# Kernel optimization log

Hardware: AMD Instinct MI355X
Metric: run time of the kernel (lower is better)

Reference implementation:

```python
import jax, jax.numpy as jnp
import numpy as np

P = 128   # input_size == proj_size
H = 512   # hidden_size
L = 6     # num_layers
STEPS = 32


def setup_inputs() -> dict:
    key = jax.random.key(0)
    ks = jax.random.split(key, 8)
    B, T = 512, 512
    scale = 1.0 / np.sqrt(H)
    s = lambda k, shape: (jax.random.normal(k, shape, jnp.float32) * scale)
    return {
        "x": jax.random.normal(ks[0], (B, T, P), jnp.float32),
        "W_ih": s(ks[1], (L, 4 * H, P)),
        "W_hh": s(ks[2], (L, 4 * H, P)),
        "b_ih": s(ks[3], (L, 4 * H)),
        "b_hh": s(ks[4], (L, 4 * H)),
        "W_hr": s(ks[5], (L, P, H)),
        "W_fc": s(ks[6], (P, P)),
        "b_fc": s(ks[7], (P,)),
    }


def _cell(xt, h, c, Wih, Whh, b, Whr):
    # PyTorch LSTM gate order: i, f, g, o ; proj: h = (o*tanh(c)) @ Whr^T
    gates = xt @ Wih.T + h @ Whh.T + b  # [B, 4H]
    i, f, g, o = jnp.split(gates, 4, axis=-1)
    c = jax.nn.sigmoid(f) * c + jax.nn.sigmoid(i) * jnp.tanh(g)
    h_full = jax.nn.sigmoid(o) * jnp.tanh(c)  # [B, H]
    h = h_full @ Whr.T  # [B, P]
    return h, c


def reference(x, W_ih, W_hh, b_ih, b_hh, W_hr, W_fc, b_fc):
    B = x.shape[0]
    b = b_ih + b_hh  # [L, 4H]
    inp = jnp.swapaxes(x, 0, 1)  # time-major [T, B, P]

    # --- encode: run full sequence through the 6-layer stack, keep final (h, c) ---
    hs, cs = [], []
    for l in range(L):
        def step(carry, xt, l=l):
            h, c = carry
            h, c = _cell(xt, h, c, W_ih[l], W_hh[l], b[l], W_hr[l])
            return (h, c), h
        init = (jnp.zeros((B, P), x.dtype), jnp.zeros((B, H), x.dtype))
        (h, c), inp = jax.lax.scan(step, init, inp)
        hs.append(h)
        cs.append(c)
    hs = jnp.stack(hs)  # [L, B, P]
    cs = jnp.stack(cs)  # [L, B, H]

    zero = jnp.zeros((B, P), x.dtype)
    def dec(carry, _):
        hs, cs = carry
        xt = zero
        nh, nc = [], []
        for l in range(L):
            h, c = _cell(xt, hs[l], cs[l], W_ih[l], W_hh[l], b[l], W_hr[l])
            nh.append(h)
            nc.append(c)
            xt = h
        out = jax.nn.sigmoid(xt) @ W_fc.T + b_fc  # sigmoid THEN fc, as in source
        return (jnp.stack(nh), jnp.stack(nc)), out

    _, zs = jax.lax.scan(dec, (hs, cs), None, length=STEPS)  # [32, B, P]
    return jnp.swapaxes(zs, 0, 1)  # [B, 32, P]
```

## Files before the change

kernel.cpp:

```cpp
#include <hip/hip_runtime.h>

typedef short s8v __attribute__((ext_vector_type(8)));
typedef float f4v __attribute__((ext_vector_type(4)));
typedef unsigned long long ull;

#define NLAYER 6
#define HID    512
#define PROJ   128
#define SEQT   512
#define BATCH  512
#define DSTEPS 32
#define TOTS   (SEQT + DSTEPS)
#define NG     2048
#define BC     64
#define NCHUNK (BATCH / BC)
#define NUNIT  (NLAYER * NCHUNK)
#define RINGP  4
#define PP_SH  8192
#define FSTRIDE 16

#define GFRAGS (NLAYER * 128 * 8 * 64)
#define PFRAGS (NLAYER * 8 * 16 * 64)
#define FFRAGS (8 * 4 * 64)
#define NFLAGS (NUNIT * 4 * FSTRIDE)

static __device__ __forceinline__ unsigned short f2b(float f) {
    union { float f; unsigned int u; } v; v.f = f;
    unsigned int r = v.u + 0x7fffu + ((v.u >> 16) & 1u);
    return (unsigned short)(r >> 16);
}
static __device__ __forceinline__ float b2f(unsigned short s) {
    union { float f; unsigned int u; } v; v.u = ((unsigned int)s) << 16;
    return v.f;
}
static __device__ __forceinline__ float sigf(float x) {
    x = fminf(fmaxf(x, -30.f), 30.f);
    return 1.f / (1.f + __expf(-x));
}
static __device__ __forceinline__ float tanh_fast(float x) {
    x = fminf(fmaxf(x, -15.f), 15.f);
    float t = __expf(-2.f * x);
    return (1.f - t) / (1.f + t);
}
static __device__ __forceinline__ f4v mfma16(s8v a, s8v b, f4v c) {
    return __builtin_amdgcn_mfma_f32_16x16x32_bf16(a, b, c, 0, 0, 0);
}
static __device__ __forceinline__ ull ald(const ull* p) {
    return __hip_atomic_load(p, __ATOMIC_RELAXED, __HIP_MEMORY_SCOPE_AGENT);
}
static __device__ __forceinline__ void spin_ge(unsigned* p, unsigned v) {
    while (__hip_atomic_load(p, __ATOMIC_RELAXED, __HIP_MEMORY_SCOPE_AGENT) < v)
        __builtin_amdgcn_s_sleep(2);
}
static __device__ __forceinline__ ull pk4(float a, float b, float c, float d) {
    return (ull)f2b(a) | ((ull)f2b(b) << 16) | ((ull)f2b(c) << 32) | ((ull)f2b(d) << 48);
}
static __device__ __forceinline__ float rsum4(ull v0, ull v1, ull v2, ull v3, int sh) {
    return b2f((unsigned short)(v0 >> sh)) + b2f((unsigned short)(v1 >> sh))
         + b2f((unsigned short)(v2 >> sh)) + b2f((unsigned short)(v3 >> sh));
}

__global__ __launch_bounds__(256) void lstm_prepack(
    const float* __restrict__ Wih, const float* __restrict__ Whh,
    const float* __restrict__ bih, const float* __restrict__ bhh,
    const float* __restrict__ Whr, const float* __restrict__ Wfc,
    const float* __restrict__ bfcin,
    unsigned short* __restrict__ gB, unsigned short* __restrict__ pB,
    unsigned short* __restrict__ fB, float* __restrict__ bsum,
    float* __restrict__ bfc, unsigned int* __restrict__ flags)
{
    int tid = blockIdx.x * 256 + threadIdx.x;

    if (tid < GFRAGS) {
        const int lane = tid & 63;
        int rest = tid >> 6;
        const int kt = rest & 7;   rest >>= 3;
        const int nt = rest & 127; rest >>= 7;
        const int l  = rest;
        const int n  = nt * 16 + (lane & 15);
        const int kb = kt * 32 + (lane >> 4) * 8;
        const float* src = (kb < 128)
            ? (Wih + ((size_t)l * NG + n) * PROJ + kb)
            : (Whh + ((size_t)l * NG + n) * PROJ + (kb - 128));
        unsigned short o[8];
        #pragma unroll
        for (int e = 0; e < 8; ++e) o[e] = f2b(src[e]);
        *(s8v*)(gB + (size_t)tid * 8) = *(const s8v*)o;
        return;
    }
    tid -= GFRAGS;
    if (tid < PFRAGS) {
        const int lane = tid & 63;
        int rest = tid >> 6;
        const int kt = rest & 15; rest >>= 4;
        const int nt = rest & 7;  rest >>= 3;
        const int l  = rest;
        const int n  = nt * 16 + (lane & 15);
        const int kb = kt * 32 + (lane >> 4) * 8;
        const float* src = Whr + ((size_t)l * PROJ + n) * HID + kb;
        unsigned short o[8];
        #pragma unroll
        for (int e = 0; e < 8; ++e) o[e] = f2b(src[e]);
        *(s8v*)(pB + (size_t)tid * 8) = *(const s8v*)o;
        return;
    }
    tid -= PFRAGS;
    if (tid < FFRAGS) {
        const int lane = tid & 63;
        int rest = tid >> 6;
        const int kt = rest & 3;
        const int nt = rest >> 2;
        const int n  = nt * 16 + (lane & 15);
        const int kb = kt * 32 + (lane >> 4) * 8;
        const float* src = Wfc + (size_t)n * PROJ + kb;
        unsigned short o[8];
        #pragma unroll
        for (int e = 0; e < 8; ++e) o[e] = f2b(src[e]);
        *(s8v*)(fB + (size_t)tid * 8) = *(const s8v*)o;
        return;
    }
    tid -= FFRAGS;
    if (tid < NLAYER * NG) { bsum[tid] = bih[tid] + bhh[tid]; return; }
    tid -= NLAYER * NG;
    if (tid < PROJ) { bfc[tid] = bfcin[tid]; return; }
    tid -= PROJ;
    if (tid < NFLAGS) { flags[tid] = 0u; return; }
}

__global__ __launch_bounds__(512) void lstm_main(
    const float* __restrict__ x,
    const unsigned short* __restrict__ gB,
    const unsigned short* __restrict__ pB,
    const unsigned short* __restrict__ fB,
    const float* __restrict__ bsum,
    const float* __restrict__ bfc,
    unsigned int* __restrict__ flags,
    unsigned short* __restrict__ pp,
    float* __restrict__ out)
{
    const int xcd  = blockIdx.x & 7;
    const int slot = blockIdx.x >> 3;
    const int uo   = slot >> 2;
    const int sub  = slot & 3;
    const int unit = xcd * 6 + uo;
    const int l    = unit >> 3;
    const int bb   = (unit & 7) * BC;

    __shared__ __align__(16) unsigned short xcat[64][264];
    __shared__ __align__(16) unsigned short hfullA[64][136];
    __shared__ __align__(16) unsigned short pslab[2048 * 8];

    const int tid  = threadIdx.x;
    const int lane = tid & 63;
    const int w    = tid >> 6;
    const int u    = sub * 8 + w;
    const int mrow = lane & 15;
    const int kgrp = lane >> 4;

    for (int i = tid; i < 64 * 264; i += 512) ((unsigned short*)xcat)[i] = 0;

    const s8v* gfrag = (const s8v*)gB;
    const s8v* pfrag = (const s8v*)pB;
    const s8v* ffrag = (const s8v*)fB;

    s8v wreg[4][8];
    #pragma unroll
    for (int g = 0; g < 4; ++g)
      #pragma unroll
      for (int kt = 0; kt < 8; ++kt)
        wreg[g][kt] = gfrag[(((size_t)l * 128 + g * 32 + u) * 8 + kt) * 64 + lane];

    float bias[4];
    #pragma unroll
    for (int g = 0; g < 4; ++g)
        bias[g] = bsum[l * NG + g * HID + u * 16 + mrow];

    for (int i = tid; i < 2048; i += 512) {
        const int nt = i >> 8, ktl = (i >> 6) & 3, ln = i & 63;
        ((s8v*)pslab)[i] = pfrag[(((size_t)l * 8 + nt) * 16 + sub * 4 + ktl) * 64 + ln];
    }

    f4v cst[4];
    #pragma unroll
    for (int mt = 0; mt < 4; ++mt) cst[mt] = (f4v){0.f, 0.f, 0.f, 0.f};

    unsigned int* tg = flags;

    __syncthreads();

    #pragma unroll 1
    for (int s = 0; s < TOTS; ++s) {
        if (s > 0 && tid < 4)
            spin_ge(&tg[(unit * 4 + tid) * FSTRIDE], (unsigned)s);
        if (l > 0 && tid >= 64 && tid < 68)
            spin_ge(&tg[((unit - NCHUNK) * 4 + (tid - 64)) * FSTRIDE], (unsigned)(s + 1));
        if (l < NLAYER - 1 && s >= RINGP && tid >= 128 && tid < 132)
            spin_ge(&tg[((unit + NCHUNK) * 4 + (tid - 128)) * FSTRIDE], (unsigned)(s - RINGP + 1));
        __syncthreads();

        if (l > 0) {
            const ull* bu = (const ull*)(pp + ((size_t)((unit - NCHUNK) * RINGP + (s & 3)) * 4) * PP_SH);
            const ull* bh = (const ull*)(pp + ((size_t)(unit * RINGP + ((s - 1) & 3)) * 4) * PP_SH);
            if (s > 0) {
                #pragma unroll
                for (int k = 0; k < 4; ++k) {
                    const int idx = k * 512 + tid;
                    const int m = idx >> 5, p4 = idx & 31;
                    const ull a0 = ald(bu + idx),        a1 = ald(bu + 2048 + idx);
                    const ull a2 = ald(bu + 4096 + idx), a3 = ald(bu + 6144 + idx);
                    const ull b0 = ald(bh + idx),        b1 = ald(bh + 2048 + idx);
                    const ull b2 = ald(bh + 4096 + idx), b3 = ald(bh + 6144 + idx);
                    *(ull*)&xcat[m][p4 * 4] = pk4(
                        rsum4(a0, a1, a2, a3, 0),  rsum4(a0, a1, a2, a3, 16),
                        rsum4(a0, a1, a2, a3, 32), rsum4(a0, a1, a2, a3, 48));
                    *(ull*)&xcat[m][128 + p4 * 4] = pk4(
                        rsum4(b0, b1, b2, b3, 0),  rsum4(b0, b1, b2, b3, 16),
                        rsum4(b0, b1, b2, b3, 32), rsum4(b0, b1, b2, b3, 48));
                }
            } else {
                #pragma unroll
                for (int k = 0; k < 4; ++k) {
                    const int idx = k * 512 + tid;
                    const int m = idx >> 5, p4 = idx & 31;
                    const ull a0 = ald(bu + idx),        a1 = ald(bu + 2048 + idx);
                    const ull a2 = ald(bu + 4096 + idx), a3 = ald(bu + 6144 + idx);
                    *(ull*)&xcat[m][p4 * 4] = pk4(
                        rsum4(a0, a1, a2, a3, 0),  rsum4(a0, a1, a2, a3, 16),
                        rsum4(a0, a1, a2, a3, 32), rsum4(a0, a1, a2, a3, 48));
                }
            }
        } else {
            if (s < SEQT) {
                #pragma unroll
                for (int k = 0; k < 4; ++k) {
                    const int f = k * 512 + tid;
                    const int m = f >> 5, q4 = f & 31;
                    const float4 v = *(const float4*)(x + (((size_t)(bb + m)) * SEQT + s) * PROJ + q4 * 4);
                    *(ull*)&xcat[m][q4 * 4] = pk4(v.x, v.y, v.z, v.w);
                }
            } else if (s == SEQT) {
                #pragma unroll
                for (int k = 0; k < 4; ++k) {
                    const int f = k * 512 + tid;
                    *(ull*)&xcat[f >> 5][(f & 31) * 4] = 0ull;
                }
            }
            if (s > 0) {
                const ull* bh = (const ull*)(pp + ((size_t)(unit * RINGP + ((s - 1) & 3)) * 4) * PP_SH);
                #pragma unroll
                for (int k = 0; k < 4; ++k) {
                    const int idx = k * 512 + tid;
                    const int m = idx >> 5, p4 = idx & 31;
                    const ull b0 = ald(bh + idx),        b1 = ald(bh + 2048 + idx);
                    const ull b2 = ald(bh + 4096 + idx), b3 = ald(bh + 6144 + idx);
                    *(ull*)&xcat[m][128 + p4 * 4] = pk4(
                        rsum4(b0, b1, b2, b3, 0),  rsum4(b0, b1, b2, b3, 16),
                        rsum4(b0, b1, b2, b3, 32), rsum4(b0, b1, b2, b3, 48));
                }
            }
        }
        __syncthreads();

        #pragma unroll
        for (int mt = 0; mt < 4; ++mt) {
            f4v a0 = (f4v){bias[0], bias[0], bias[0], bias[0]};
            f4v a1 = (f4v){bias[1], bias[1], bias[1], bias[1]};
            f4v a2 = (f4v){bias[2], bias[2], bias[2], bias[2]};
            f4v a3 = (f4v){bias[3], bias[3], bias[3], bias[3]};
            #pragma unroll
            for (int kt = 0; kt < 8; ++kt) {
                const s8v a = *(const s8v*)&xcat[mt * 16 + mrow][kt * 32 + kgrp * 8];
                a0 = mfma16(a, wreg[0][kt], a0);
                a1 = mfma16(a, wreg[1][kt], a1);
                a2 = mfma16(a, wreg[2][kt], a2);
                a3 = mfma16(a, wreg[3][kt], a3);
            }
            f4v cv = cst[mt];
            #pragma unroll
            for (int r = 0; r < 4; ++r) {
                const float cn = sigf(a1[r]) * cv[r] + sigf(a0[r]) * tanh_fast(a2[r]);
                const float hf = sigf(a3[r]) * tanh_fast(cn);
                cv[r] = cn;
                hfullA[mt * 16 + kgrp * 4 + r][w * 16 + mrow] = f2b(hf);
            }
            cst[mt] = cv;
        }
        __syncthreads();

        {
            f4v pacc[4];
            #pragma unroll
            for (int mt = 0; mt < 4; ++mt) pacc[mt] = (f4v){0.f, 0.f, 0.f, 0.f};
            #pragma unroll
            for (int ktl = 0; ktl < 4; ++ktl) {
                const s8v wf = ((const s8v*)pslab)[(w * 4 + ktl) * 64 + lane];
                #pragma unroll
                for (int mt = 0; mt < 4; ++mt) {
                    const s8v hf = *(const s8v*)&hfullA[mt * 16 + mrow][ktl * 32 + kgrp * 8];
                    pacc[mt] = mfma16(wf, hf, pacc[mt]);
                }
            }
            unsigned short* dst = pp + ((size_t)(unit * RINGP + (s & 3)) * 4 + sub) * PP_SH;
            #pragma unroll
            for (int mt = 0; mt < 4; ++mt) {
                ull* p8 = (ull*)(dst + (mt * 16 + mrow) * 128 + w * 16 + kgrp * 4);
                __hip_atomic_store(p8, pk4(pacc[mt][0], pacc[mt][1], pacc[mt][2], pacc[mt][3]),
                                   __ATOMIC_RELAXED, __HIP_MEMORY_SCOPE_AGENT);
            }
        }
        __syncthreads();
        if (tid == 0)
            __hip_atomic_store(&tg[(unit * 4 + sub) * FSTRIDE], (unsigned)(s + 1),
                               __ATOMIC_RELAXED, __HIP_MEMORY_SCOPE_AGENT);

        if (l == NLAYER - 1 && s >= SEQT) {
            if (tid < 4) spin_ge(&tg[(unit * 4 + tid) * FSTRIDE], (unsigned)(s + 1));
            __syncthreads();
            const ull* bh = (const ull*)(pp + ((size_t)(unit * RINGP + (s & 3)) * 4) * PP_SH);
            #pragma unroll
            for (int k = 0; k < 4; ++k) {
                const int idx = k * 512 + tid;
                const int m = idx >> 5, p4 = idx & 31;
                const ull b0 = ald(bh + idx),        b1 = ald(bh + 2048 + idx);
                const ull b2 = ald(bh + 4096 + idx), b3 = ald(bh + 6144 + idx);
                *(ull*)&hfullA[m][p4 * 4] = pk4(
                    sigf(rsum4(b0, b1, b2, b3, 0)),  sigf(rsum4(b0, b1, b2, b3, 16)),
                    sigf(rsum4(b0, b1, b2, b3, 32)), sigf(rsum4(b0, b1, b2, b3, 48)));
            }
            __syncthreads();
            const float bv = bfc[w * 16 + mrow];
            f4v facc[4];
            #pragma unroll
            for (int mt = 0; mt < 4; ++mt) facc[mt] = (f4v){bv, bv, bv, bv};
            #pragma unroll
            for (int kt = 0; kt < 4; ++kt) {
                const s8v bf = ffrag[((size_t)w * 4 + kt) * 64 + lane];
                #pragma unroll
                for (int mt = 0; mt < 4; ++mt) {
                    const s8v a = *(const s8v*)&hfullA[mt * 16 + mrow][kt * 32 + kgrp * 8];
                    facc[mt] = mfma16(a, bf, facc[mt]);
                }
            }
            const int td = s - SEQT;
            #pragma unroll
            for (int mt = 0; mt < 4; ++mt)
                #pragma unroll
                for (int r = 0; r < 4; ++r)
                    out[(((size_t)(bb + mt * 16 + kgrp * 4 + r)) * DSTEPS + td) * PROJ
                        + w * 16 + mrow] = facc[mt][r];
        }
    }
}

extern "C" void kernel_launch(void* const* d_in, const int* in_sizes, int n_in,
                              void* d_out, int out_size, void* d_ws, size_t ws_size,
                              hipStream_t stream)
{
    const float* x    = (const float*)d_in[0];
    const float* Wih  = (const float*)d_in[1];
    const float* Whh  = (const float*)d_in[2];
    const float* bih  = (const float*)d_in[3];
    const float* bhh  = (const float*)d_in[4];
    const float* Whr  = (const float*)d_in[5];
    const float* Wfc  = (const float*)d_in[6];
    const float* bfcv = (const float*)d_in[7];

    char* ws = (char*)d_ws;
    size_t off = 0;
    auto alloc = [&](size_t b) { char* p = ws + off; off += (b + 255) & ~(size_t)255; return p; };
    unsigned short* gB  = (unsigned short*)alloc((size_t)GFRAGS * 16);
    unsigned short* pB  = (unsigned short*)alloc((size_t)PFRAGS * 16);
    unsigned short* fB  = (unsigned short*)alloc((size_t)FFRAGS * 16);
    float* bsum         = (float*)alloc((size_t)NLAYER * NG * 4);
    float* bfc          = (float*)alloc((size_t)PROJ * 4);
    unsigned int* flags = (unsigned int*)alloc((size_t)NFLAGS * 4);
    unsigned short* pp  = (unsigned short*)alloc((size_t)NUNIT * RINGP * 4 * PP_SH * 2);
    if (off > ws_size) return;

    const int total = GFRAGS + PFRAGS + FFRAGS + NLAYER * NG + PROJ + NFLAGS;
    lstm_prepack<<<(total + 255) / 256, 256, 0, stream>>>(
        Wih, Whh, bih, bhh, Whr, Wfc, bfcv, gB, pB, fB, bsum, bfc, flags);
    lstm_main<<<NUNIT * 4, 512, 0, stream>>>(
        x, gB, pB, fB, bsum, bfc, flags, pp, (float*)d_out);
}
```

Baseline: 7.086 ms.

## Split each timestep into two batch-half phases with separate readiness flags

Each time step is split into two phases, each handling half of the 64-row batch chunk, and each phase has its own set of progress flags. Downstream layers and the next step can begin on the first half as soon as it is published, instead of waiting for the whole chunk. This deepens the wavefront pipeline across layers and sub-blocks. The cost is twice as many barriers, spin-waits and flag stores per step, and each phase does half the MFMA work, which lowers per-phase efficiency.

New measurement: 7.094 ms. About the same (+0.1%).

```diff
diff --git a/kernel.cpp b/kernel.cpp
--- a/kernel.cpp
+++ b/kernel.cpp
@@ -18,11 +18,12 @@
 #define RINGP  4
 #define PP_SH  8192
 #define FSTRIDE 16
+#define TAGHALF (NUNIT * 4 * FSTRIDE)
 
 #define GFRAGS (NLAYER * 128 * 8 * 64)
 #define PFRAGS (NLAYER * 8 * 16 * 64)
 #define FFRAGS (8 * 4 * 64)
-#define NFLAGS (NUNIT * 4 * FSTRIDE)
+#define NFLAGS (2 * TAGHALF)
 
 static __device__ __forceinline__ unsigned short f2b(float f) {
     union { float f; unsigned int u; } v; v.f = f;
@@ -190,131 +191,142 @@
 
     #pragma unroll 1
     for (int s = 0; s < TOTS; ++s) {
-        if (s > 0 && tid < 4)
-            spin_ge(&tg[(unit * 4 + tid) * FSTRIDE], (unsigned)s);
-        if (l > 0 && tid >= 64 && tid < 68)
-            spin_ge(&tg[((unit - NCHUNK) * 4 + (tid - 64)) * FSTRIDE], (unsigned)(s + 1));
-        if (l < NLAYER - 1 && s >= RINGP && tid >= 128 && tid < 132)
-            spin_ge(&tg[((unit + NCHUNK) * 4 + (tid - 128)) * FSTRIDE], (unsigned)(s - RINGP + 1));
-        __syncthreads();
-
-        if (l > 0) {
-            const ull* bu = (const ull*)(pp + ((size_t)((unit - NCHUNK) * RINGP + (s & 3)) * 4) * PP_SH);
-            const ull* bh = (const ull*)(pp + ((size_t)(unit * RINGP + ((s - 1) & 3)) * 4) * PP_SH);
-            if (s > 0) {
-                #pragma unroll
-                for (int k = 0; k < 4; ++k) {
-                    const int idx = k * 512 + tid;
-                    const int m = idx >> 5, p4 = idx & 31;
-                    const ull a0 = ald(bu + idx),        a1 = ald(bu + 2048 + idx);
-                    const ull a2 = ald(bu + 4096 + idx), a3 = ald(bu + 6144 + idx);
-                    const ull b0 = ald(bh + idx),        b1 = ald(bh + 2048 + idx);
-                    const ull b2 = ald(bh + 4096 + idx), b3 = ald(bh + 6144 + idx);
-                    *(ull*)&xcat[m][p4 * 4] = pk4(
-                        rsum4(a0, a1, a2, a3, 0),  rsum4(a0, a1, a2, a3, 16),
-                        rsum4(a0, a1, a2, a3, 32), rsum4(a0, a1, a2, a3, 48));
-                    *(ull*)&xcat[m][128 + p4 * 4] = pk4(
-                        rsum4(b0, b1, b2, b3, 0),  rsum4(b0, b1, b2, b3, 16),
-                        rsum4(b0, b1, b2, b3, 32), rsum4(b0, b1, b2, b3, 48));
+        #pragma unroll
+        for (int ph = 0; ph < 2; ++ph) {
+            unsigned int* tgP = tg + ph * TAGHALF;
+
+            if (s > 0 && tid < 4)
+                spin_ge(&tgP[(unit * 4 + tid) * FSTRIDE], (unsigned)s);
+            if (l > 0 && tid >= 64 && tid < 68)
+                spin_ge(&tgP[((unit - NCHUNK) * 4 + (tid - 64)) * FSTRIDE], (unsigned)(s + 1));
+            if (l < NLAYER - 1 && s >= RINGP && tid >= 128 && tid < 132)
+                spin_ge(&tgP[((unit + NCHUNK) * 4 + (tid - 128)) * FSTRIDE], (unsigned)(s - RINGP + 1));
+            __syncthreads();
+
+            if (l > 0) {
+                const ull* bu = (const ull*)(pp + ((size_t)((unit - NCHUNK) * RINGP + (s & 3)) * 4) * PP_SH);
+                const ull* bh = (const ull*)(pp + ((size_t)(unit * RINGP + ((s - 1) & 3)) * 4) * PP_SH);
+                if (s > 0) {
+                    #pragma unroll
+                    for (int kk = 0; kk < 2; ++kk) {
+                        const int idx = (ph * 2 + kk) * 512 + tid;
+                        const int m = idx >> 5, p4 = idx & 31;
+                        const ull a0 = ald(bu + idx),        a1 = ald(bu + 2048 + idx);
+                        const ull a2 = ald(bu + 4096 + idx), a3 = ald(bu + 6144 + idx);
+                        const ull b0 = ald(bh + idx),        b1 = ald(bh + 2048 + idx);
+                        const ull b2 = ald(bh + 4096 + idx), b3 = ald(bh + 6144 + idx);
+                        *(ull*)&xcat[m][p4 * 4] = pk4(
+                            rsum4(a0, a1, a2, a3, 0),  rsum4(a0, a1, a2, a3, 16),
+                            rsum4(a0, a1, a2, a3, 32), rsum4(a0, a1, a2, a3, 48));
+                        *(ull*)&xcat[m][128 + p4 * 4] = pk4(
+                            rsum4(b0, b1, b2, b3, 0),  rsum4(b0, b1, b2, b3, 16),
+                            rsum4(b0, b1, b2, b3, 32), rsum4(b0, b1, b2, b3, 48));
+                    }
+                } else {
+                    #pragma unroll
+                    for (int kk = 0; kk < 2; ++kk) {
+                        const int idx = (ph * 2 + kk) * 512 + tid;
+                        const int m = idx >> 5, p4 = idx & 31;
+                        const ull a0 = ald(bu + idx),        a1 = ald(bu + 2048 + idx);
+                        const ull a2 = ald(bu + 4096 + idx), a3 = ald(bu + 6144 + idx);
+                        *(ull*)&xcat[m][p4 * 4] = pk4(
+                            rsum4(a0, a1, a2, a3, 0),  rsum4(a0, a1, a2, a3, 16),
+                            rsum4(a0, a1, a2, a3, 32), rsum4(a0, a1, a2, a3, 48));
+                    }
                 }
             } else {
-                #pragma unroll
-                for (int k = 0; k < 4; ++k) {
-                    const int idx = k * 512 + tid;
-                    const int m = idx >> 5, p4 = idx & 31;
-                    const ull a0 = ald(bu + idx),        a1 = ald(bu + 2048 + idx);
-                    const ull a2 = ald(bu + 4096 + idx), a3 = ald(bu + 6144 + idx);
-                    *(ull*)&xcat[m][p4 * 4] = pk4(
-                        rsum4(a0, a1, a2, a3, 0),  rsum4(a0, a1, a2, a3, 16),
-                        rsum4(a0, a1, a2, a3, 32), rsum4(a0, a1, a2, a3, 48));
-                }
-            }
-        } else {
-            if (s < SEQT) {
-                #pragma unroll
-                for (int k = 0; k < 4; ++k) {
-                    const int f = k * 512 + tid;
-                    const int m = f >> 5, q4 = f & 31;
-                    const float4 v = *(const float4*)(x + (((size_t)(bb + m)) * SEQT + s) * PROJ + q4 * 4);
-                    *(ull*)&xcat[m][q4 * 4] = pk4(v.x, v.y, v.z, v.w);
-                }
-            } else if (s == SEQT) {
-                #pragma unroll
-                for (int k = 0; k < 4; ++k) {
-                    const int f = k * 512 + tid;
-                    *(ull*)&xcat[f >> 5][(f & 31) * 4] = 0ull;
-                }
-            }
-            if (s > 0) {
-                const ull* bh = (const ull*)(pp + ((size_t)(unit * RINGP + ((s - 1) & 3)) * 4) * PP_SH);
-                #pragma unroll
-                for (int k = 0; k < 4; ++k) {
-                    const int idx = k * 512 + tid;
-                    const int m = idx >> 5, p4 = idx & 31;
-                    const ull b0 = ald(bh + idx),        b1 = ald(bh + 2048 + idx);
-                    const ull b2 = ald(bh + 4096 + idx), b3 = ald(bh + 6144 + idx);
-                    *(ull*)&xcat[m][128 + p4 * 4] = pk4(
-                        rsum4(b0, b1, b2, b3, 0),  rsum4(b0, b1, b2, b3, 16),
-                        rsum4(b0, b1, b2, b3, 32), rsum4(b0, b1, b2, b3, 48));
-                }
-            }
+                if (s < SEQT) {
+                    #pragma unroll
+                    for (int kk = 0; kk < 2; ++kk) {
+                        const int f = (ph * 2 + kk) * 512 + tid;
+                        const int m = f >> 5, q4 = f & 31;
+                        const float4 v = *(const float4*)(x + (((size_t)(bb + m)) * SEQT + s) * PROJ + q4 * 4);
+                        *(ull*)&xcat[m][q4 * 4] = pk4(v.x, v.y, v.z, v.w);
+                    }
+                } else if (s == SEQT) {
+                    #pragma unroll
+                    for (int kk = 0; kk < 2; ++kk) {
+                        const int f = (ph * 2 + kk) * 512 + tid;
+                        *(ull*)&xcat[f >> 5][(f & 31) * 4] = 0ull;
+                    }
+                }
+                if (s > 0) {
+                    const ull* bh = (const ull*)(pp + ((size_t)(unit * RINGP + ((s - 1) & 3)) * 4) * PP_SH);
+                    #pragma unroll
+                    for (int kk = 0; kk < 2; ++kk) {
+                        const int idx = (ph * 2 + kk) * 512 + tid;
+                        const int m = idx >> 5, p4 = idx & 31;
+                        const ull b0 = ald(bh + idx),        b1 = ald(bh + 2048 + idx);
+                        const ull b2 = ald(bh + 4096 + idx), b3 = ald(bh + 6144 + idx);
+                        *(ull*)&xcat[m][128 + p4 * 4] = pk4(
+                            rsum4(b0, b1, b2, b3, 0),  rsum4(b0, b1, b2, b3, 16),
+                            rsum4(b0, b1, b2, b3, 32), rsum4(b0, b1, b2, b3, 48));
+                    }
+                }
+            }
+            __syncthreads();
+
+            #pragma unroll
+            for (int mm = 0; mm < 2; ++mm) {
+                const int mt = ph * 2 + mm;
+                f4v a0 = (f4v){bias[0], bias[0], bias[0], bias[0]};
+                f4v a1 = (f4v){bias[1], bias[1], bias[1], bias[1]};
+                f4v a2 = (f4v){bias[2], bias[2], bias[2], bias[2]};
+                f4v a3 = (f4v){bias[3], bias[3], bias[3], bias[3]};
+                #pragma unroll
+                for (int kt = 0; kt < 8; ++kt) {
+                    const s8v a = *(const s8v*)&xcat[mt * 16 + mrow][kt * 32 + kgrp * 8];
+                    a0 = mfma16(a, wreg[0][kt], a0);
+                    a1 = mfma16(a, wreg[1][kt], a1);
+                    a2 = mfma16(a, wreg[2][kt], a2);
+                    a3 = mfma16(a, wreg[3][kt], a3);
+                }
+                f4v cv = cst[mt];
+                #pragma unroll
+                for (int r = 0; r < 4; ++r) {
+                    const float cn = sigf(a1[r]) * cv[r] + sigf(a0[r]) * tanh_fast(a2[r]);
+                    const float hf = sigf(a3[r]) * tanh_fast(cn);
+                    cv[r] = cn;
+                    hfullA[mt * 16 + kgrp * 4 + r][w * 16 + mrow] = f2b(hf);
+                }
+                cst[mt] = cv;
+            }
+            __syncthreads();
+
+            {
+                f4v pacc[2];
+                pacc[0] = (f4v){0.f, 0.f, 0.f, 0.f};
+                pacc[1] = (f4v){0.f, 0.f, 0.f, 0.f};
+                #pragma unroll
+                for (int ktl = 0; ktl < 4; ++ktl) {
+                    const s8v wf = ((const s8v*)pslab)[(w * 4 + ktl) * 64 + lane];
+                    #pragma unroll
+                    for (int mm = 0; mm < 2; ++mm) {
+                        const int mt = ph * 2 + mm;
+                        const s8v hf = *(const s8v*)&hfullA[mt * 16 + mrow][ktl * 32 + kgrp * 8];
+                        pacc[mm] = mfma16(wf, hf, pacc[mm]);
+                    }
+                }
+                unsigned short* dst = pp + ((size_t)(unit * RINGP + (s & 3)) * 4 + sub) * PP_SH;
+                #pragma unroll
+                for (int mm = 0; mm < 2; ++mm) {
+                    const int mt = ph * 2 + mm;
+                    ull* p8 = (ull*)(dst + (mt * 16 + mrow) * 128 + w * 16 + kgrp * 4);
+                    __hip_atomic_store(p8, pk4(pacc[mm][0], pacc[mm][1], pacc[mm][2], pacc[mm][3]),
+                                       __ATOMIC_RELAXED, __HIP_MEMORY_SCOPE_AGENT);
+                }
+            }
+            __syncthreads();
+            if (tid == 0)
+                __hip_atomic_store(&tgP[(unit * 4 + sub) * FSTRIDE], (unsigned)(s + 1),
+                                   __ATOMIC_RELAXED, __HIP_MEMORY_SCOPE_AGENT);
         }
-        __syncthreads();
-
-        #pragma unroll
-        for (int mt = 0; mt < 4; ++mt) {
-            f4v a0 = (f4v){bias[0], bias[0], bias[0], bias[0]};
-            f4v a1 = (f4v){bias[1], bias[1], bias[1], bias[1]};
-            f4v a2 = (f4v){bias[2], bias[2], bias[2], bias[2]};
-            f4v a3 = (f4v){bias[3], bias[3], bias[3], bias[3]};
-            #pragma unroll
-            for (int kt = 0; kt < 8; ++kt) {
-                const s8v a = *(const s8v*)&xcat[mt * 16 + mrow][kt * 32 + kgrp * 8];
-                a0 = mfma16(a, wreg[0][kt], a0);
-                a1 = mfma16(a, wreg[1][kt], a1);
-                a2 = mfma16(a, wreg[2][kt], a2);
-                a3 = mfma16(a, wreg[3][kt], a3);
-            }
-            f4v cv = cst[mt];
-            #pragma unroll
-            for (int r = 0; r < 4; ++r) {
-                const float cn = sigf(a1[r]) * cv[r] + sigf(a0[r]) * tanh_fast(a2[r]);
-                const float hf = sigf(a3[r]) * tanh_fast(cn);
-                cv[r] = cn;
-                hfullA[mt * 16 + kgrp * 4 + r][w * 16 + mrow] = f2b(hf);
-            }
-            cst[mt] = cv;
-        }
-        __syncthreads();
-
-        {
-            f4v pacc[4];
-            #pragma unroll
-            for (int mt = 0; mt < 4; ++mt) pacc[mt] = (f4v){0.f, 0.f, 0.f, 0.f};
-            #pragma unroll
-            for (int ktl = 0; ktl < 4; ++ktl) {
-                const s8v wf = ((const s8v*)pslab)[(w * 4 + ktl) * 64 + lane];
-                #pragma unroll
-                for (int mt = 0; mt < 4; ++mt) {
-                    const s8v hf = *(const s8v*)&hfullA[mt * 16 + mrow][ktl * 32 + kgrp * 8];
-                    pacc[mt] = mfma16(wf, hf, pacc[mt]);
-                }
-            }
-            unsigned short* dst = pp + ((size_t)(unit * RINGP + (s & 3)) * 4 + sub) * PP_SH;
-            #pragma unroll
-            for (int mt = 0; mt < 4; ++mt) {
-                ull* p8 = (ull*)(dst + (mt * 16 + mrow) * 128 + w * 16 + kgrp * 4);
-                __hip_atomic_store(p8, pk4(pacc[mt][0], pacc[mt][1], pacc[mt][2], pacc[mt][3]),
-                                   __ATOMIC_RELAXED, __HIP_MEMORY_SCOPE_AGENT);
-            }
-        }
-        __syncthreads();
-        if (tid == 0)
-            __hip_atomic_store(&tg[(unit * 4 + sub) * FSTRIDE], (unsigned)(s + 1),
-                               __ATOMIC_RELAXED, __HIP_MEMORY_SCOPE_AGENT);
 
         if (l == NLAYER - 1 && s >= SEQT) {
-            if (tid < 4) spin_ge(&tg[(unit * 4 + tid) * FSTRIDE], (unsigned)(s + 1));
+            if (tid < 8) {
+                unsigned int* tp = tg + (tid >> 2) * TAGHALF;
+                spin_ge(&tp[(unit * 4 + (tid & 3)) * FSTRIDE], (unsigned)(s + 1));
+            }
             __syncthreads();
             const ull* bh = (const ull*)(pp + ((size_t)(unit * RINGP + (s & 3)) * 4) * PP_SH);
             #pragma unroll
```

## Vectorize partial-projection exchange with 16-byte coherent loads/stores in new layout

Applied to the files above, without the earlier changes.

Changes the layout of the per-step projection partial sums in the global ring buffer so that each thread writes two 16-byte stores and each reader issues eight 16-byte loads, replacing many 8-byte atomic loads and stores. The loads use inline asm with cache-bypass bits and explicit waitcnts, so the h-path loads overlap the reduction of the upper-layer input. It also adds a min-blocks hint to launch_bounds. The aim is to cut latency on the critical inter-block communication path, at the cost of hand-written asm memory ordering that relies on the sc0/sc1 semantics for coherence.

New measurement: 6.956 ms. No clear change (-1.8%).

```diff
diff --git a/kernel.cpp b/kernel.cpp
--- a/kernel.cpp
+++ b/kernel.cpp
@@ -2,6 +2,7 @@
 
 typedef short s8v __attribute__((ext_vector_type(8)));
 typedef float f4v __attribute__((ext_vector_type(4)));
+typedef unsigned int u4v __attribute__((ext_vector_type(4)));
 typedef unsigned long long ull;
 
 #define NLAYER 6
@@ -29,9 +30,11 @@
     unsigned int r = v.u + 0x7fffu + ((v.u >> 16) & 1u);
     return (unsigned short)(r >> 16);
 }
-static __device__ __forceinline__ float b2f(unsigned short s) {
-    union { float f; unsigned int u; } v; v.u = ((unsigned int)s) << 16;
-    return v.f;
+static __device__ __forceinline__ float blo(unsigned int u) {
+    union { unsigned int x; float f; } v; v.x = u << 16; return v.f;
+}
+static __device__ __forceinline__ float bhi(unsigned int u) {
+    union { unsigned int x; float f; } v; v.x = u & 0xffff0000u; return v.f;
 }
 static __device__ __forceinline__ float sigf(float x) {
     x = fminf(fmaxf(x, -30.f), 30.f);
@@ -45,9 +48,6 @@
 static __device__ __forceinline__ f4v mfma16(s8v a, s8v b, f4v c) {
     return __builtin_amdgcn_mfma_f32_16x16x32_bf16(a, b, c, 0, 0, 0);
 }
-static __device__ __forceinline__ ull ald(const ull* p) {
-    return __hip_atomic_load(p, __ATOMIC_RELAXED, __HIP_MEMORY_SCOPE_AGENT);
-}
 static __device__ __forceinline__ void spin_ge(unsigned* p, unsigned v) {
     while (__hip_atomic_load(p, __ATOMIC_RELAXED, __HIP_MEMORY_SCOPE_AGENT) < v)
         __builtin_amdgcn_s_sleep(2);
@@ -55,9 +55,62 @@
 static __device__ __forceinline__ ull pk4(float a, float b, float c, float d) {
     return (ull)f2b(a) | ((ull)f2b(b) << 16) | ((ull)f2b(c) << 32) | ((ull)f2b(d) << 48);
 }
-static __device__ __forceinline__ float rsum4(ull v0, ull v1, ull v2, ull v3, int sh) {
-    return b2f((unsigned short)(v0 >> sh)) + b2f((unsigned short)(v1 >> sh))
-         + b2f((unsigned short)(v2 >> sh)) + b2f((unsigned short)(v3 >> sh));
+static __device__ __forceinline__ ull red4(unsigned a0, unsigned a1, unsigned a2, unsigned a3,
+                                           unsigned b0, unsigned b1, unsigned b2, unsigned b3) {
+    return pk4(blo(a0) + blo(a1) + blo(a2) + blo(a3),
+               bhi(a0) + bhi(a1) + bhi(a2) + bhi(a3),
+               blo(b0) + blo(b1) + blo(b2) + blo(b3),
+               bhi(b0) + bhi(b1) + bhi(b2) + bhi(b3));
+}
+static __device__ __forceinline__ ull red4s(unsigned a0, unsigned a1, unsigned a2, unsigned a3,
+                                            unsigned b0, unsigned b1, unsigned b2, unsigned b3) {
+    return pk4(sigf(blo(a0) + blo(a1) + blo(a2) + blo(a3)),
+               sigf(bhi(a0) + bhi(a1) + bhi(a2) + bhi(a3)),
+               sigf(blo(b0) + blo(b1) + blo(b2) + blo(b3)),
+               sigf(bhi(b0) + bhi(b1) + bhi(b2) + bhi(b3)));
+}
+static __device__ __forceinline__ u4v mk4(ull a, ull b) {
+    u4v r; r.x = (unsigned)a; r.y = (unsigned)(a >> 32);
+    r.z = (unsigned)b; r.w = (unsigned)(b >> 32); return r;
+}
+
+#define LD8_BODY(WAITSTR) \
+    const ull* p0 = b;        const ull* p1 = b + 2;    \
+    const ull* p2 = b + 2048; const ull* p3 = b + 2050; \
+    const ull* p4 = b + 4096; const ull* p5 = b + 4098; \
+    const ull* p6 = b + 6144; const ull* p7 = b + 6146; \
+    asm volatile( \
+        "global_load_dwordx4 %0, %8, off sc0 sc1\n\t"  \
+        "global_load_dwordx4 %1, %9, off sc0 sc1\n\t"  \
+        "global_load_dwordx4 %2, %10, off sc0 sc1\n\t" \
+        "global_load_dwordx4 %3, %11, off sc0 sc1\n\t" \
+        "global_load_dwordx4 %4, %12, off sc0 sc1\n\t" \
+        "global_load_dwordx4 %5, %13, off sc0 sc1\n\t" \
+        "global_load_dwordx4 %6, %14, off sc0 sc1\n\t" \
+        "global_load_dwordx4 %7, %15, off sc0 sc1"     \
+        WAITSTR \
+        : "=&v"(r0), "=&v"(r1), "=&v"(r2), "=&v"(r3), \
+          "=&v"(r4), "=&v"(r5), "=&v"(r6), "=&v"(r7)  \
+        : "v"(p0), "v"(p1), "v"(p2), "v"(p3), "v"(p4), "v"(p5), "v"(p6), "v"(p7) \
+        : "memory")
+
+static __device__ __forceinline__ void ld8nw(const ull* b,
+    u4v& r0, u4v& r1, u4v& r2, u4v& r3, u4v& r4, u4v& r5, u4v& r6, u4v& r7) {
+    LD8_BODY("");
+}
+static __device__ __forceinline__ void ld8w8(const ull* b,
+    u4v& r0, u4v& r1, u4v& r2, u4v& r3, u4v& r4, u4v& r5, u4v& r6, u4v& r7) {
+    LD8_BODY("\n\ts_waitcnt vmcnt(8)");
+}
+static __device__ __forceinline__ void ld8w0(const ull* b,
+    u4v& r0, u4v& r1, u4v& r2, u4v& r3, u4v& r4, u4v& r5, u4v& r6, u4v& r7) {
+    LD8_BODY("\n\ts_waitcnt vmcnt(0)");
+}
+static __device__ __forceinline__ void st16x2(ull* p, u4v v01, u4v v23) {
+    asm volatile("global_store_dwordx4 %0, %2, off sc0 sc1\n\t"
+                 "global_store_dwordx4 %1, %3, off sc0 sc1\n\t"
+                 "s_waitcnt vmcnt(0)"
+                 :: "v"(p), "v"(p + 2), "v"(v01), "v"(v23) : "memory");
 }
 
 __global__ __launch_bounds__(256) void lstm_prepack(
@@ -127,7 +180,7 @@
     if (tid < NFLAGS) { flags[tid] = 0u; return; }
 }
 
-__global__ __launch_bounds__(512) void lstm_main(
+__global__ __launch_bounds__(512, 2) void lstm_main(
     const float* __restrict__ x,
     const unsigned short* __restrict__ gB,
     const unsigned short* __restrict__ pB,
@@ -156,6 +209,8 @@
     const int u    = sub * 8 + w;
     const int mrow = lane & 15;
     const int kgrp = lane >> 4;
+    const int mrc  = tid >> 5;
+    const int pc4  = (tid & 31) * 4;
 
     for (int i = tid; i < 64 * 264; i += 512) ((unsigned short*)xcat)[i] = 0;
 
@@ -199,35 +254,31 @@
         __syncthreads();
 
         if (l > 0) {
-            const ull* bu = (const ull*)(pp + ((size_t)((unit - NCHUNK) * RINGP + (s & 3)) * 4) * PP_SH);
-            const ull* bh = (const ull*)(pp + ((size_t)(unit * RINGP + ((s - 1) & 3)) * 4) * PP_SH);
+            const ull* bu = (const ull*)(pp + ((size_t)((unit - NCHUNK) * RINGP + (s & 3)) * 4) * PP_SH) + tid * 4;
             if (s > 0) {
-                #pragma unroll
-                for (int k = 0; k < 4; ++k) {
-                    const int idx = k * 512 + tid;
-                    const int m = idx >> 5, p4 = idx & 31;
-                    const ull a0 = ald(bu + idx),        a1 = ald(bu + 2048 + idx);
-                    const ull a2 = ald(bu + 4096 + idx), a3 = ald(bu + 6144 + idx);
-                    const ull b0 = ald(bh + idx),        b1 = ald(bh + 2048 + idx);
-                    const ull b2 = ald(bh + 4096 + idx), b3 = ald(bh + 6144 + idx);
-                    *(ull*)&xcat[m][p4 * 4] = pk4(
-                        rsum4(a0, a1, a2, a3, 0),  rsum4(a0, a1, a2, a3, 16),
-                        rsum4(a0, a1, a2, a3, 32), rsum4(a0, a1, a2, a3, 48));
-                    *(ull*)&xcat[m][128 + p4 * 4] = pk4(
-                        rsum4(b0, b1, b2, b3, 0),  rsum4(b0, b1, b2, b3, 16),
-                        rsum4(b0, b1, b2, b3, 32), rsum4(b0, b1, b2, b3, 48));
-                }
+                const ull* bh = (const ull*)(pp + ((size_t)(unit * RINGP + ((s - 1) & 3)) * 4) * PP_SH) + tid * 4;
+                u4v a0, a1, a2, a3, a4, a5, a6, a7, c0, c1, c2, c3, c4, c5, c6, c7;
+                ld8nw(bu, a0, a1, a2, a3, a4, a5, a6, a7);
+                ld8w8(bh, c0, c1, c2, c3, c4, c5, c6, c7);
+                __builtin_amdgcn_sched_barrier(0);
+                *(ull*)&xcat[     mrc][pc4] = red4(a0.x, a2.x, a4.x, a6.x, a0.y, a2.y, a4.y, a6.y);
+                *(ull*)&xcat[16 + mrc][pc4] = red4(a0.z, a2.z, a4.z, a6.z, a0.w, a2.w, a4.w, a6.w);
+                *(ull*)&xcat[32 + mrc][pc4] = red4(a1.x, a3.x, a5.x, a7.x, a1.y, a3.y, a5.y, a7.y);
+                *(ull*)&xcat[48 + mrc][pc4] = red4(a1.z, a3.z, a5.z, a7.z, a1.w, a3.w, a5.w, a7.w);
+                asm volatile("s_waitcnt vmcnt(0)" ::: "memory");
+                __builtin_amdgcn_sched_barrier(0);
+                *(ull*)&xcat[     mrc][128 + pc4] = red4(c0.x, c2.x, c4.x, c6.x, c0.y, c2.y, c4.y, c6.y);
+                *(ull*)&xcat[16 + mrc][128 + pc4] = red4(c0.z, c2.z, c4.z, c6.z, c0.w, c2.w, c4.w, c6.w);
+                *(ull*)&xcat[32 + mrc][128 + pc4] = red4(c1.x, c3.x, c5.x, c7.x, c1.y, c3.y, c5.y, c7.y);
+                *(ull*)&xcat[48 + mrc][128 + pc4] = red4(c1.z, c3.z, c5.z, c7.z, c1.w, c3.w, c5.w, c7.w);
             } else {
-                #pragma unroll
-                for (int k = 0; k < 4; ++k) {
-                    const int idx = k * 512 + tid;
-                    const int m = idx >> 5, p4 = idx & 31;
-                    const ull a0 = ald(bu + idx),        a1 = ald(bu + 2048 + idx);
-                    const ull a2 = ald(bu + 4096 + idx), a3 = ald(bu + 6144 + idx);
-                    *(ull*)&xcat[m][p4 * 4] = pk4(
-                        rsum4(a0, a1, a2, a3, 0),  rsum4(a0, a1, a2, a3, 16),
-                        rsum4(a0, a1, a2, a3, 32), rsum4(a0, a1, a2, a3, 48));
-                }
+                u4v a0, a1, a2, a3, a4, a5, a6, a7;
+                ld8w0(bu, a0, a1, a2, a3, a4, a5, a6, a7);
+                __builtin_amdgcn_sched_barrier(0);
+                *(ull*)&xcat[     mrc][pc4] = red4(a0.x, a2.x, a4.x, a6.x, a0.y, a2.y, a4.y, a6.y);
+                *(ull*)&xcat[16 + mrc][pc4] = red4(a0.z, a2.z, a4.z, a6.z, a0.w, a2.w, a4.w, a6.w);
+                *(ull*)&xcat[32 + mrc][pc4] = red4(a1.x, a3.x, a5.x, a7.x, a1.y, a3.y, a5.y, a7.y);
+                *(ull*)&xcat[48 + mrc][pc4] = red4(a1.z, a3.z, a5.z, a7.z, a1.w, a3.w, a5.w, a7.w);
             }
         } else {
             if (s < SEQT) {
@@ -246,17 +297,14 @@
                 }
             }
             if (s > 0) {
-                const ull* bh = (const ull*)(pp + ((size_t)(unit * RINGP + ((s - 1) & 3)) * 4) * PP_SH);
-                #pragma unroll
-                for (int k = 0; k < 4; ++k) {
-                    const int idx = k * 512 + tid;
-                    const int m = idx >> 5, p4 = idx & 31;
-                    const ull b0 = ald(bh + idx),        b1 = ald(bh + 2048 + idx);
-                    const ull b2 = ald(bh + 4096 + idx), b3 = ald(bh + 6144 + idx);
-                    *(ull*)&xcat[m][128 + p4 * 4] = pk4(
-                        rsum4(b0, b1, b2, b3, 0),  rsum4(b0, b1, b2, b3, 16),
-                        rsum4(b0, b1, b2, b3, 32), rsum4(b0, b1, b2, b3, 48));
-                }
+                const ull* bh = (const ull*)(pp + ((size_t)(unit * RINGP + ((s - 1) & 3)) * 4) * PP_SH) + tid * 4;
+                u4v c0, c1, c2, c3, c4, c5, c6, c7;
+                ld8w0(bh, c0, c1, c2, c3, c4, c5, c6, c7);
+                __builtin_amdgcn_sched_barrier(0);
+                *(ull*)&xcat[     mrc][128 + pc4] = red4(c0.x, c2.x, c4.x, c6.x, c0.y, c2.y, c4.y, c6.y);
+                *(ull*)&xcat[16 + mrc][128 + pc4] = red4(c0.z, c2.z, c4.z, c6.z, c0.w, c2.w, c4.w, c6.w);
+                *(ull*)&xcat[32 + mrc][128 + pc4] = red4(c1.x, c3.x, c5.x, c7.x, c1.y, c3.y, c5.y, c7.y);
+                *(ull*)&xcat[48 + mrc][128 + pc4] = red4(c1.z, c3.z, c5.z, c7.z, c1.w, c3.w, c5.w, c7.w);
             }
         }
         __syncthreads();
@@ -300,13 +348,13 @@
                     pacc[mt] = mfma16(wf, hf, pacc[mt]);
                 }
             }
-            unsigned short* dst = pp + ((size_t)(unit * RINGP + (s & 3)) * 4 + sub) * PP_SH;
-            #pragma unroll
-            for (int mt = 0; mt < 4; ++mt) {
-                ull* p8 = (ull*)(dst + (mt * 16 + mrow) * 128 + w * 16 + kgrp * 4);
-                __hip_atomic_store(p8, pk4(pacc[mt][0], pacc[mt][1], pacc[mt][2], pacc[mt][3]),
-                                   __ATOMIC_RELAXED, __HIP_MEMORY_SCOPE_AGENT);
-            }
+            ull* dst = (ull*)(pp + ((size_t)(unit * RINGP + (s & 3)) * 4 + sub) * PP_SH)
+                       + ((size_t)mrow * 32 + w * 4 + kgrp) * 4;
+            st16x2(dst,
+                   mk4(pk4(pacc[0][0], pacc[0][1], pacc[0][2], pacc[0][3]),
+                       pk4(pacc[1][0], pacc[1][1], pacc[1][2], pacc[1][3])),
+                   mk4(pk4(pacc[2][0], pacc[2][1], pacc[2][2], pacc[2][3]),
+                       pk4(pacc[3][0], pacc[3][1], pacc[3][2], pacc[3][3])));
         }
         __syncthreads();
         if (tid == 0)
@@ -316,17 +364,14 @@
         if (l == NLAYER - 1 && s >= SEQT) {
             if (tid < 4) spin_ge(&tg[(unit * 4 + tid) * FSTRIDE], (unsigned)(s + 1));
             __syncthreads();
-            const ull* bh = (const ull*)(pp + ((size_t)(unit * RINGP + (s & 3)) * 4) * PP_SH);
-            #pragma unroll
-            for (int k = 0; k < 4; ++k) {
-                const int idx = k * 512 + tid;
-                const int m = idx >> 5, p4 = idx & 31;
-                const ull b0 = ald(bh + idx),        b1 = ald(bh + 2048 + idx);
-                const ull b2 = ald(bh + 4096 + idx), b3 = ald(bh + 6144 + idx);
-                *(ull*)&hfullA[m][p4 * 4] = pk4(
-                    sigf(rsum4(b0, b1, b2, b3, 0)),  sigf(rsum4(b0, b1, b2, b3, 16)),
-                    sigf(rsum4(b0, b1, b2, b3, 32)), sigf(rsum4(b0, b1, b2, b3, 48)));
-            }
+            const ull* bh = (const ull*)(pp + ((size_t)(unit * RINGP + (s & 3)) * 4) * PP_SH) + tid * 4;
+            u4v a0, a1, a2, a3, a4, a5, a6, a7;
+            ld8w0(bh, a0, a1, a2, a3, a4, a5, a6, a7);
+            __builtin_amdgcn_sched_barrier(0);
+            *(ull*)&hfullA[     mrc][pc4] = red4s(a0.x, a2.x, a4.x, a6.x, a0.y, a2.y, a4.y, a6.y);
+            *(ull*)&hfullA[16 + mrc][pc4] = red4s(a0.z, a2.z, a4.z, a6.z, a0.w, a2.w, a4.w, a6.w);
+            *(ull*)&hfullA[32 + mrc][pc4] = red4s(a1.x, a3.x, a5.x, a7.x, a1.y, a3.y, a5.y, a7.y);
+            *(ull*)&hfullA[48 + mrc][pc4] = red4s(a1.z, a3.z, a5.z, a7.z, a1.w, a3.w, a5.w, a7.w);
             __syncthreads();
             const float bv = bfc[w * 16 + mrow];
             f4v facc[4];
```
